# Optimization experiments

Measured on AMD Instinct MI355X. Metric: run time of the kernel, lower is better.

## Reference

```python
import jax, jax.numpy as jnp
import numpy as np

N = 100000
E = 1600000
F_IN = 512
HID = 64
N_CLASSES = 16


def setup_inputs() -> dict:
    key = jax.random.key(0)
    k0, k1, k2, k3 = jax.random.split(key, 4)
    features = jax.random.normal(k0, (N, F_IN), dtype=jnp.float32)
    edge_idx = jax.random.randint(k1, (2, E), 0, N, dtype=jnp.int64)
    # Glorot-style init matching torch_geometric GCNConv defaults
    W1 = jax.random.normal(k2, (F_IN, HID), dtype=jnp.float32) * (1.0 / np.sqrt(F_IN))
    b1 = jnp.zeros((HID,), dtype=jnp.float32)
    W2 = jax.random.normal(k3, (HID, N_CLASSES), dtype=jnp.float32) * (1.0 / np.sqrt(HID))
    b2 = jnp.zeros((N_CLASSES,), dtype=jnp.float32)
    return {"features": features, "edge_idx": edge_idx, "W1": W1, "b1": b1, "W2": W2, "b2": b2}


def _gcn_layer(x, row, col, norm, W, b):
    # Linear transform first (out_channels < in_channels -> cheaper messages)
    h = x @ W                                   # [N, out]
    msg = h[row] * norm[:, None]                # gather + scale, [E+N, out]
    out = jax.ops.segment_sum(msg, col, num_segments=x.shape[0])  # scatter-add
    return out + b


def reference(features, edge_idx, W1, b1, W2, b2):
    n = features.shape[0]
    loop = jnp.arange(n, dtype=edge_idx.dtype)
    row = jnp.concatenate([edge_idx[0], loop])  # sources (+ self-loops)
    col = jnp.concatenate([edge_idx[1], loop])  # targets (+ self-loops)
    w = jnp.ones(row.shape[0], dtype=features.dtype)  # edge_weight=None -> ones
    # Symmetric normalization D^{-1/2} A D^{-1/2} (degree over targets)
    deg = jax.ops.segment_sum(w, col, num_segments=n)
    dinv = jnp.where(deg > 0, deg ** -0.5, 0.0)
    norm = dinv[row] * w * dinv[col]            # [E+N]

    x = jax.nn.relu(_gcn_layer(features, row, col, norm, W1, b1))
    # Dropout: eval mode (identity)
    logits = _gcn_layer(x, row, col, norm, W2, b2)
    return logits
```

## Files before the change

kernel.cpp:

```cpp
#include <hip/hip_runtime.h>

#define NN 100000
#define EE 1600000
#define FIN 512
#define HID 64
#define NC 16
#define ELLW 64
#define CPAD 16

#define KB_ 196
#define BCAP 10240
#define S1E 2048

typedef __attribute__((ext_vector_type(8))) short bf16x8;
typedef __attribute__((ext_vector_type(4))) float f32x4;

__device__ __forceinline__ unsigned short f2bf(float f) {
    union { float f; unsigned u; } v; v.f = f;
    unsigned r = v.u + 0x7FFFu + ((v.u >> 16) & 1u);
    return (unsigned short)(r >> 16);
}
__device__ __forceinline__ float asf(unsigned u) {
    union { unsigned u; float f; } v; v.u = u; return v.f;
}

__global__ void k_zero(unsigned* __restrict__ p, int n) {
    int i = blockIdx.x * blockDim.x + threadIdx.x;
    if (i < n) p[i] = 0u;
}

__global__ __launch_bounds__(256) void k_bin(
    const int* __restrict__ erow, const int* __restrict__ ecol,
    unsigned* __restrict__ gcur, unsigned* __restrict__ staged) {
    __shared__ unsigned hist[256];
    __shared__ unsigned scanb[256];
    __shared__ unsigned cur[256];
    __shared__ unsigned sbase[256];
    __shared__ unsigned pk[S1E];
    __shared__ unsigned ga[S1E];
    const int t = threadIdx.x;
    const int e0 = blockIdx.x * S1E;

    hist[t] = 0;
    cur[t] = 0;
    __syncthreads();

    unsigned pkd[8];
    int bs[8];
#pragma unroll
    for (int i = 0; i < 8; ++i) {
        int e = e0 + i * 256 + t;
        if (e < EE) {
            int c = ecol[e];
            int src = erow[e];
            int b = c >> 9;
            bs[i] = b;
            pkd[i] = (unsigned)src | ((unsigned)(c & 511) << 17);
            atomicAdd(&hist[b], 1u);
        } else {
            bs[i] = -1;
        }
    }
    __syncthreads();
    scanb[t] = hist[t];
    __syncthreads();
    for (int d = 1; d < 256; d <<= 1) {
        unsigned add = (t >= d) ? scanb[t - d] : 0u;
        __syncthreads();
        scanb[t] += add;
        __syncthreads();
    }
    if (t < KB_ && hist[t] > 0) sbase[t] = atomicAdd(&gcur[(size_t)t * CPAD], hist[t]);
    __syncthreads();
#pragma unroll
    for (int i = 0; i < 8; ++i) {
        int b = bs[i];
        if (b >= 0) {
            unsigned ls = atomicAdd(&cur[b], 1u);
            unsigned pos = scanb[b] - hist[b] + ls;
            unsigned gp = sbase[b] + ls;
            pk[pos] = pkd[i];
            ga[pos] = (gp < BCAP) ? ((unsigned)b * BCAP + gp) : 0xFFFFFFFFu;
        }
    }
    __syncthreads();
    unsigned tot = scanb[255];
#pragma unroll
    for (int i = 0; i < 8; ++i) {
        unsigned idx = i * 256 + t;
        if (idx < tot && ga[idx] != 0xFFFFFFFFu) staged[ga[idx]] = pk[idx];
    }
}

__global__ __launch_bounds__(256) void k_scat2(
    const unsigned* __restrict__ gcur, const unsigned* __restrict__ staged,
    int* __restrict__ ell, unsigned* __restrict__ cnt, float* __restrict__ dinv) {
    __shared__ unsigned lcnt[512];
    const int t = threadIdx.x;
    const int b = blockIdx.x;
    lcnt[t] = 0; lcnt[t + 256] = 0;
    __syncthreads();
    unsigned n = gcur[(size_t)b * CPAD];
    if (n > BCAP) n = BCAP;
    const unsigned base = (unsigned)b * BCAP;
    const int node0 = b << 9;
    for (unsigned idx = t; idx < n; idx += 256) {
        unsigned p = staged[base + idx];
        int src = (int)(p & 0x1FFFFu);
        int dl = (int)(p >> 17);
        unsigned slot = atomicAdd(&lcnt[dl], 1u);
        if (slot < ELLW) ell[(size_t)(node0 + dl) * ELLW + slot] = src;
    }
    __syncthreads();
#pragma unroll
    for (int i = 0; i < 2; ++i) {
        int dl = i * 256 + t;
        int node = node0 + dl;
        if (node < NN) {
            unsigned c = lcnt[dl];
            cnt[node] = c;
            dinv[node] = 1.0f / sqrtf((float)(c + 1u));
        }
    }
}

__global__ void k_prepw(const float* __restrict__ W1, unsigned short* __restrict__ W1t) {
    int id = blockIdx.x * blockDim.x + threadIdx.x;
    if (id >= HID * FIN) return;
    int c = id >> 9;
    int k = id & 511;
    W1t[id] = f2bf(W1[(size_t)k * HID + c]);
}

#define BM 128
#define BK 64

__global__ __launch_bounds__(256) void k_gemm1(
    const float* __restrict__ A, const unsigned short* __restrict__ W1t,
    const float* __restrict__ dinv, unsigned short* __restrict__ h1s) {
    __shared__ unsigned short sA[BM * BK];
    __shared__ unsigned short sB[HID * BK];
    const int t = threadIdx.x;
    const int w = t >> 6;
    const int l = t & 63;
    const int row0 = blockIdx.x * BM;

    f32x4 acc[2][4];
#pragma unroll
    for (int fr = 0; fr < 2; ++fr)
#pragma unroll
        for (int fc = 0; fc < 4; ++fc)
            acc[fr][fc] = (f32x4){0.f, 0.f, 0.f, 0.f};

    for (int kb = 0; kb < FIN; kb += BK) {
        __syncthreads();
#pragma unroll
        for (int i = 0; i < 4; ++i) {
            int idx = i * 256 + t;
            int r = idx >> 3, g = idx & 7;
            float4 v0 = {0.f, 0.f, 0.f, 0.f}, v1 = {0.f, 0.f, 0.f, 0.f};
            if (row0 + r < NN) {
                const float* p = &A[(size_t)(row0 + r) * FIN + kb + g * 8];
                v0 = *reinterpret_cast<const float4*>(p);
                v1 = *reinterpret_cast<const float4*>(p + 4);
            }
            unsigned short tmp[8] = {f2bf(v0.x), f2bf(v0.y), f2bf(v0.z), f2bf(v0.w),
                                     f2bf(v1.x), f2bf(v1.y), f2bf(v1.z), f2bf(v1.w)};
            *reinterpret_cast<uint4*>((char*)sA + r * 128 + ((g ^ (r & 7)) << 4)) =
                *reinterpret_cast<uint4*>(tmp);
        }
#pragma unroll
        for (int i = 0; i < 2; ++i) {
            int idx = i * 256 + t;
            int c = idx >> 3, g = idx & 7;
            uint4 v = *reinterpret_cast<const uint4*>(&W1t[(size_t)c * FIN + kb + g * 8]);
            *reinterpret_cast<uint4*>((char*)sB + c * 128 + ((g ^ (c & 7)) << 4)) = v;
        }
        __syncthreads();
#pragma unroll
        for (int ks = 0; ks < 2; ++ks) {
            const int gk = ks * 4 + (l >> 4);
            bf16x8 a[2], b[4];
#pragma unroll
            for (int fr = 0; fr < 2; ++fr) {
                int r = w * 32 + fr * 16 + (l & 15);
                a[fr] = *reinterpret_cast<const bf16x8*>((char*)sA + r * 128 + ((gk ^ (r & 7)) << 4));
            }
#pragma unroll
            for (int fc = 0; fc < 4; ++fc) {
                int c = fc * 16 + (l & 15);
                b[fc] = *reinterpret_cast<const bf16x8*>((char*)sB + c * 128 + ((gk ^ (c & 7)) << 4));
            }
#pragma unroll
            for (int fr = 0; fr < 2; ++fr)
#pragma unroll
                for (int fc = 0; fc < 4; ++fc)
                    acc[fr][fc] = __builtin_amdgcn_mfma_f32_16x16x32_bf16(
                        a[fr], b[fc], acc[fr][fc], 0, 0, 0);
        }
    }
#pragma unroll
    for (int fr = 0; fr < 2; ++fr) {
#pragma unroll
        for (int r = 0; r < 4; ++r) {
            int grow = row0 + w * 32 + fr * 16 + (l >> 4) * 4 + r;
            if (grow >= NN) continue;
            float di = dinv[grow];
#pragma unroll
            for (int fc = 0; fc < 4; ++fc) {
                int col = fc * 16 + (l & 15);
                h1s[(size_t)grow * HID + col] = f2bf(acc[fr][fc][r] * di);
            }
        }
    }
}

__global__ __launch_bounds__(256) void k_agg1(
    const unsigned* __restrict__ cnt, const int* __restrict__ ell,
    const unsigned short* __restrict__ h1s, const float* __restrict__ dinv,
    const float* __restrict__ b1, unsigned short* __restrict__ x) {
    int wid = (blockIdx.x * blockDim.x + threadIdx.x) >> 6;
    if (wid >= NN) return;
    const int l = threadIdx.x & 63;
    const int g = l >> 3;
    const int q = l & 7;
    const int total = (int)cnt[wid] + 1;
    const int base = wid * ELLW;

    float a0 = 0.f, a1 = 0.f, a2 = 0.f, a3 = 0.f;
    float a4 = 0.f, a5 = 0.f, a6 = 0.f, a7 = 0.f;
    for (int s = 0; s < total; s += 8) {
        int e = s + g;
        int ee = min(e, total - 1);
        int src = (ee == 0) ? wid : ell[base + ee - 1];
        uint4 u = *reinterpret_cast<const uint4*>(&h1s[(size_t)src * HID + q * 8]);
        float m = (e < total) ? 1.f : 0.f;
        a0 = fmaf(m, asf(u.x << 16), a0);
        a1 = fmaf(m, asf(u.x & 0xFFFF0000u), a1);
        a2 = fmaf(m, asf(u.y << 16), a2);
        a3 = fmaf(m, asf(u.y & 0xFFFF0000u), a3);
        a4 = fmaf(m, asf(u.z << 16), a4);
        a5 = fmaf(m, asf(u.z & 0xFFFF0000u), a5);
        a6 = fmaf(m, asf(u.w << 16), a6);
        a7 = fmaf(m, asf(u.w & 0xFFFF0000u), a7);
    }
#pragma unroll
    for (int d = 8; d <= 32; d <<= 1) {
        a0 += __shfl_xor(a0, d); a1 += __shfl_xor(a1, d);
        a2 += __shfl_xor(a2, d); a3 += __shfl_xor(a3, d);
        a4 += __shfl_xor(a4, d); a5 += __shfl_xor(a5, d);
        a6 += __shfl_xor(a6, d); a7 += __shfl_xor(a7, d);
    }
    if (g == 0) {
        float di = dinv[wid];
        float4 bA = *reinterpret_cast<const float4*>(&b1[q * 8]);
        float4 bB = *reinterpret_cast<const float4*>(&b1[q * 8 + 4]);
        float r0 = fmaxf(fmaf(a0, di, bA.x), 0.f);
        float r1 = fmaxf(fmaf(a1, di, bA.y), 0.f);
        float r2 = fmaxf(fmaf(a2, di, bA.z), 0.f);
        float r3 = fmaxf(fmaf(a3, di, bA.w), 0.f);
        float r4 = fmaxf(fmaf(a4, di, bB.x), 0.f);
        float r5 = fmaxf(fmaf(a5, di, bB.y), 0.f);
        float r6 = fmaxf(fmaf(a6, di, bB.z), 0.f);
        float r7 = fmaxf(fmaf(a7, di, bB.w), 0.f);
        uint4 pv;
        pv.x = (unsigned)f2bf(r0) | ((unsigned)f2bf(r1) << 16);
        pv.y = (unsigned)f2bf(r2) | ((unsigned)f2bf(r3) << 16);
        pv.z = (unsigned)f2bf(r4) | ((unsigned)f2bf(r5) << 16);
        pv.w = (unsigned)f2bf(r6) | ((unsigned)f2bf(r7) << 16);
        *reinterpret_cast<uint4*>(&x[(size_t)wid * HID + q * 8]) = pv;
    }
}

__global__ __launch_bounds__(256) void k_gemm2(
    const unsigned short* __restrict__ x, const float* __restrict__ W2,
    const float* __restrict__ dinv, unsigned short* __restrict__ h2s) {
    __shared__ float sW[HID][NC];
    const int t = threadIdx.x;
#pragma unroll
    for (int i = 0; i < 4; ++i) {
        int q = t + i * 256;
        sW[q >> 4][q & 15] = W2[q];
    }
    __syncthreads();
    int i = blockIdx.x * blockDim.x + t;
    if (i >= NN) return;

    float acc[NC];
#pragma unroll
    for (int j = 0; j < NC; ++j) acc[j] = 0.f;
    const unsigned short* xr = &x[(size_t)i * HID];
#pragma unroll
    for (int k8 = 0; k8 < 8; ++k8) {
        uint4 u = *reinterpret_cast<const uint4*>(&xr[k8 * 8]);
        float f[8] = {asf(u.x << 16), asf(u.x & 0xFFFF0000u),
                      asf(u.y << 16), asf(u.y & 0xFFFF0000u),
                      asf(u.z << 16), asf(u.z & 0xFFFF0000u),
                      asf(u.w << 16), asf(u.w & 0xFFFF0000u)};
#pragma unroll
        for (int m = 0; m < 8; ++m)
#pragma unroll
            for (int j = 0; j < NC; ++j)
                acc[j] = fmaf(f[m], sW[k8 * 8 + m][j], acc[j]);
    }
    float di = dinv[i];
    unsigned short hv[NC];
#pragma unroll
    for (int j = 0; j < NC; ++j) hv[j] = f2bf(acc[j] * di);
    *reinterpret_cast<uint4*>(&h2s[(size_t)i * NC])     = *reinterpret_cast<uint4*>(hv);
    *reinterpret_cast<uint4*>(&h2s[(size_t)i * NC + 8]) = *reinterpret_cast<uint4*>(hv + 8);
}

__global__ __launch_bounds__(256) void k_agg2(
    const unsigned* __restrict__ cnt, const int* __restrict__ ell,
    const unsigned short* __restrict__ h2s, const float* __restrict__ dinv,
    const float* __restrict__ b2, float* __restrict__ out) {
    int wid = (blockIdx.x * blockDim.x + threadIdx.x) >> 6;
    if (wid >= NN) return;
    const int l = threadIdx.x & 63;
    const int g = l >> 1;
    const int q = l & 1;
    const int total = (int)cnt[wid] + 1;
    const int base = wid * ELLW;

    float a0 = 0.f, a1 = 0.f, a2 = 0.f, a3 = 0.f;
    float a4 = 0.f, a5 = 0.f, a6 = 0.f, a7 = 0.f;
    for (int s = 0; s < total; s += 32) {
        int e = s + g;
        int ee = min(e, total - 1);
        int src = (ee == 0) ? wid : ell[base + ee - 1];
        uint4 u = *reinterpret_cast<const uint4*>(&h2s[(size_t)src * NC + q * 8]);
        float m = (e < total) ? 1.f : 0.f;
        a0 = fmaf(m, asf(u.x << 16), a0);
        a1 = fmaf(m, asf(u.x & 0xFFFF0000u), a1);
        a2 = fmaf(m, asf(u.y << 16), a2);
        a3 = fmaf(m, asf(u.y & 0xFFFF0000u), a3);
        a4 = fmaf(m, asf(u.z << 16), a4);
        a5 = fmaf(m, asf(u.z & 0xFFFF0000u), a5);
        a6 = fmaf(m, asf(u.w << 16), a6);
        a7 = fmaf(m, asf(u.w & 0xFFFF0000u), a7);
    }
#pragma unroll
    for (int d = 2; d <= 32; d <<= 1) {
        a0 += __shfl_xor(a0, d); a1 += __shfl_xor(a1, d);
        a2 += __shfl_xor(a2, d); a3 += __shfl_xor(a3, d);
        a4 += __shfl_xor(a4, d); a5 += __shfl_xor(a5, d);
        a6 += __shfl_xor(a6, d); a7 += __shfl_xor(a7, d);
    }
    if (g == 0) {
        float di = dinv[wid];
        float4 bA = *reinterpret_cast<const float4*>(&b2[q * 8]);
        float4 bB = *reinterpret_cast<const float4*>(&b2[q * 8 + 4]);
        float4 w0, w1;
        w0.x = fmaf(a0, di, bA.x); w0.y = fmaf(a1, di, bA.y);
        w0.z = fmaf(a2, di, bA.z); w0.w = fmaf(a3, di, bA.w);
        w1.x = fmaf(a4, di, bB.x); w1.y = fmaf(a5, di, bB.y);
        w1.z = fmaf(a6, di, bB.z); w1.w = fmaf(a7, di, bB.w);
        *reinterpret_cast<float4*>(&out[(size_t)wid * NC + q * 8])     = w0;
        *reinterpret_cast<float4*>(&out[(size_t)wid * NC + q * 8 + 4]) = w1;
    }
}

extern "C" void kernel_launch(void* const* d_in, const int* in_sizes, int n_in,
                              void* d_out, int out_size, void* d_ws, size_t ws_size,
                              hipStream_t stream) {
    const float* features = (const float*)d_in[0];
    const int*   edges    = (const int*)d_in[1];
    const float* W1       = (const float*)d_in[2];
    const float* b1       = (const float*)d_in[3];
    const float* W2       = (const float*)d_in[4];
    const float* b2       = (const float*)d_in[5];
    float* out = (float*)d_out;

    const int* erow = edges;
    const int* ecol = edges + EE;

    char* ws = (char*)d_ws;
    size_t o = 0;
    auto alloc = [&](size_t bytes) { size_t p = o; o = (o + bytes + 255) & ~255ULL; return p; };
    unsigned*       gcur  = (unsigned*)      (ws + alloc((size_t)KB_ * CPAD * 4));
    unsigned*       cnt   = (unsigned*)      (ws + alloc((size_t)NN * 4));
    float*          dinv  = (float*)         (ws + alloc((size_t)NN * 4));
    unsigned*       staged= (unsigned*)      (ws + alloc((size_t)KB_ * BCAP * 4));
    unsigned short* W1t   = (unsigned short*)(ws + alloc((size_t)HID * FIN * 2));
    int*            ell   = (int*)           (ws + alloc((size_t)(KB_ << 9) * ELLW * 4));
    unsigned short* h1s   = (unsigned short*)(ws + alloc((size_t)NN * HID * 2));
    unsigned short* x     = (unsigned short*)(ws + alloc((size_t)NN * HID * 2));
    unsigned short* h2s   = (unsigned short*)(ws + alloc((size_t)NN * NC * 2));

    k_zero<<<(KB_ * CPAD + 255) / 256, 256, 0, stream>>>(gcur, KB_ * CPAD);
    k_prepw<<<(HID * FIN + 255) / 256, 256, 0, stream>>>(W1, W1t);
    k_bin<<<(EE + S1E - 1) / S1E, 256, 0, stream>>>(erow, ecol, gcur, staged);
    k_scat2<<<KB_, 256, 0, stream>>>(gcur, staged, ell, cnt, dinv);

    k_gemm1<<<(NN + BM - 1) / BM, 256, 0, stream>>>(features, W1t, dinv, h1s);
    k_agg1 <<<NN / 4, 256, 0, stream>>>(cnt, ell, h1s, dinv, b1, x);

    k_gemm2<<<(NN + 255) / 256, 256, 0, stream>>>(x, W2, dinv, h2s);
    k_agg2 <<<NN / 4, 256, 0, stream>>>(cnt, ell, h2s, dinv, b2, out);
}
```

Measured before the change: 188.2 us.

## Overlap GEMM1 with edge binning via heterogeneous fused launches

The source-side dinv scaling moves out of GEMM1 and into the aggregation gather, so GEMM1 no longer depends on the graph degree computation. GEMM1 blocks are then split across two launches that also run the binning and scatter stages, letting the feature GEMM overlap the graph-structure preprocessing. The zero and weight-prep kernels are merged into one init kernel. In exchange, agg1 does an extra dinv[src] load per edge, shared memory is sized for the larger of the two block bodies, and bf16 rounding of h1 now happens before the dinv scaling rather than after.

After: 198.6 us. +5.5%, slower.

```diff
diff --git a/kernel.cpp b/kernel.cpp
--- a/kernel.cpp
+++ b/kernel.cpp
@@ -11,6 +11,10 @@
 #define KB_ 196
 #define BCAP 10240
 #define S1E 2048
+#define NBIN 782
+#define GA 391
+#define GB 391
+#define SMEM_BYTES 24576
 
 typedef __attribute__((ext_vector_type(8))) short bf16x8;
 typedef __attribute__((ext_vector_type(4))) float f32x4;
@@ -24,126 +28,29 @@
     union { unsigned u; float f; } v; v.u = u; return v.f;
 }
 
-__global__ void k_zero(unsigned* __restrict__ p, int n) {
-    int i = blockIdx.x * blockDim.x + threadIdx.x;
-    if (i < n) p[i] = 0u;
-}
-
-__global__ __launch_bounds__(256) void k_bin(
-    const int* __restrict__ erow, const int* __restrict__ ecol,
-    unsigned* __restrict__ gcur, unsigned* __restrict__ staged) {
-    __shared__ unsigned hist[256];
-    __shared__ unsigned scanb[256];
-    __shared__ unsigned cur[256];
-    __shared__ unsigned sbase[256];
-    __shared__ unsigned pk[S1E];
-    __shared__ unsigned ga[S1E];
-    const int t = threadIdx.x;
-    const int e0 = blockIdx.x * S1E;
-
-    hist[t] = 0;
-    cur[t] = 0;
-    __syncthreads();
-
-    unsigned pkd[8];
-    int bs[8];
-#pragma unroll
-    for (int i = 0; i < 8; ++i) {
-        int e = e0 + i * 256 + t;
-        if (e < EE) {
-            int c = ecol[e];
-            int src = erow[e];
-            int b = c >> 9;
-            bs[i] = b;
-            pkd[i] = (unsigned)src | ((unsigned)(c & 511) << 17);
-            atomicAdd(&hist[b], 1u);
-        } else {
-            bs[i] = -1;
-        }
-    }
-    __syncthreads();
-    scanb[t] = hist[t];
-    __syncthreads();
-    for (int d = 1; d < 256; d <<= 1) {
-        unsigned add = (t >= d) ? scanb[t - d] : 0u;
-        __syncthreads();
-        scanb[t] += add;
-        __syncthreads();
-    }
-    if (t < KB_ && hist[t] > 0) sbase[t] = atomicAdd(&gcur[(size_t)t * CPAD], hist[t]);
-    __syncthreads();
-#pragma unroll
-    for (int i = 0; i < 8; ++i) {
-        int b = bs[i];
-        if (b >= 0) {
-            unsigned ls = atomicAdd(&cur[b], 1u);
-            unsigned pos = scanb[b] - hist[b] + ls;
-            unsigned gp = sbase[b] + ls;
-            pk[pos] = pkd[i];
-            ga[pos] = (gp < BCAP) ? ((unsigned)b * BCAP + gp) : 0xFFFFFFFFu;
-        }
-    }
-    __syncthreads();
-    unsigned tot = scanb[255];
-#pragma unroll
-    for (int i = 0; i < 8; ++i) {
-        unsigned idx = i * 256 + t;
-        if (idx < tot && ga[idx] != 0xFFFFFFFFu) staged[ga[idx]] = pk[idx];
-    }
-}
-
-__global__ __launch_bounds__(256) void k_scat2(
-    const unsigned* __restrict__ gcur, const unsigned* __restrict__ staged,
-    int* __restrict__ ell, unsigned* __restrict__ cnt, float* __restrict__ dinv) {
-    __shared__ unsigned lcnt[512];
-    const int t = threadIdx.x;
-    const int b = blockIdx.x;
-    lcnt[t] = 0; lcnt[t + 256] = 0;
-    __syncthreads();
-    unsigned n = gcur[(size_t)b * CPAD];
-    if (n > BCAP) n = BCAP;
-    const unsigned base = (unsigned)b * BCAP;
-    const int node0 = b << 9;
-    for (unsigned idx = t; idx < n; idx += 256) {
-        unsigned p = staged[base + idx];
-        int src = (int)(p & 0x1FFFFu);
-        int dl = (int)(p >> 17);
-        unsigned slot = atomicAdd(&lcnt[dl], 1u);
-        if (slot < ELLW) ell[(size_t)(node0 + dl) * ELLW + slot] = src;
-    }
-    __syncthreads();
-#pragma unroll
-    for (int i = 0; i < 2; ++i) {
-        int dl = i * 256 + t;
-        int node = node0 + dl;
-        if (node < NN) {
-            unsigned c = lcnt[dl];
-            cnt[node] = c;
-            dinv[node] = 1.0f / sqrtf((float)(c + 1u));
-        }
-    }
-}
-
-__global__ void k_prepw(const float* __restrict__ W1, unsigned short* __restrict__ W1t) {
+__global__ void k_init(const float* __restrict__ W1, unsigned short* __restrict__ W1t,
+                       unsigned* __restrict__ gcur) {
     int id = blockIdx.x * blockDim.x + threadIdx.x;
-    if (id >= HID * FIN) return;
-    int c = id >> 9;
-    int k = id & 511;
-    W1t[id] = f2bf(W1[(size_t)k * HID + c]);
+    if (id < KB_ * CPAD) gcur[id] = 0u;
+    if (id < HID * FIN) {
+        int c = id >> 9;
+        int k = id & 511;
+        W1t[id] = f2bf(W1[(size_t)k * HID + c]);
+    }
 }
 
 #define BM 128
 #define BK 64
 
-__global__ __launch_bounds__(256) void k_gemm1(
-    const float* __restrict__ A, const unsigned short* __restrict__ W1t,
-    const float* __restrict__ dinv, unsigned short* __restrict__ h1s) {
-    __shared__ unsigned short sA[BM * BK];
-    __shared__ unsigned short sB[HID * BK];
+__device__ __forceinline__ void gemm1_body(
+    char* smem, int blk, const float* __restrict__ A,
+    const unsigned short* __restrict__ W1t, unsigned short* __restrict__ h1s) {
+    unsigned short* sA = (unsigned short*)smem;
+    unsigned short* sB = (unsigned short*)(smem + BM * BK * 2);
     const int t = threadIdx.x;
     const int w = t >> 6;
     const int l = t & 63;
-    const int row0 = blockIdx.x * BM;
+    const int row0 = blk * BM;
 
     f32x4 acc[2][4];
 #pragma unroll
@@ -205,14 +112,127 @@
         for (int r = 0; r < 4; ++r) {
             int grow = row0 + w * 32 + fr * 16 + (l >> 4) * 4 + r;
             if (grow >= NN) continue;
-            float di = dinv[grow];
 #pragma unroll
             for (int fc = 0; fc < 4; ++fc) {
                 int col = fc * 16 + (l & 15);
-                h1s[(size_t)grow * HID + col] = f2bf(acc[fr][fc][r] * di);
+                h1s[(size_t)grow * HID + col] = f2bf(acc[fr][fc][r]);
             }
         }
     }
+}
+
+__device__ __forceinline__ void bin_body(
+    char* smem, int bb, const int* __restrict__ erow, const int* __restrict__ ecol,
+    unsigned* __restrict__ gcur, unsigned* __restrict__ staged) {
+    unsigned* hist  = (unsigned*)smem;
+    unsigned* scanb = hist + 256;
+    unsigned* cur   = scanb + 256;
+    unsigned* sbase = cur + 256;
+    unsigned* pk    = sbase + 256;
+    unsigned* ga    = pk + S1E;
+    const int t = threadIdx.x;
+    const int e0 = bb * S1E;
+
+    hist[t] = 0;
+    cur[t] = 0;
+    __syncthreads();
+
+    unsigned pkd[8];
+    int bs[8];
+#pragma unroll
+    for (int i = 0; i < 8; ++i) {
+        int e = e0 + i * 256 + t;
+        if (e < EE) {
+            int c = ecol[e];
+            int src = erow[e];
+            int b = c >> 9;
+            bs[i] = b;
+            pkd[i] = (unsigned)src | ((unsigned)(c & 511) << 17);
+            atomicAdd(&hist[b], 1u);
+        } else {
+            bs[i] = -1;
+        }
+    }
+    __syncthreads();
+    scanb[t] = hist[t];
+    __syncthreads();
+    for (int d = 1; d < 256; d <<= 1) {
+        unsigned add = (t >= d) ? scanb[t - d] : 0u;
+        __syncthreads();
+        scanb[t] += add;
+        __syncthreads();
+    }
+    if (t < KB_ && hist[t] > 0) sbase[t] = atomicAdd(&gcur[(size_t)t * CPAD], hist[t]);
+    __syncthreads();
+#pragma unroll
+    for (int i = 0; i < 8; ++i) {
+        int b = bs[i];
+        if (b >= 0) {
+            unsigned ls = atomicAdd(&cur[b], 1u);
+            unsigned pos = scanb[b] - hist[b] + ls;
+            unsigned gp = sbase[b] + ls;
+            pk[pos] = pkd[i];
+            ga[pos] = (gp < BCAP) ? ((unsigned)b * BCAP + gp) : 0xFFFFFFFFu;
+        }
+    }
+    __syncthreads();
+    unsigned tot = scanb[255];
+#pragma unroll
+    for (int i = 0; i < 8; ++i) {
+        unsigned idx = i * 256 + t;
+        if (idx < tot && ga[idx] != 0xFFFFFFFFu) staged[ga[idx]] = pk[idx];
+    }
+}
+
+__device__ __forceinline__ void scat2_body(
+    char* smem, int b, const unsigned* __restrict__ gcur, const unsigned* __restrict__ staged,
+    int* __restrict__ ell, unsigned* __restrict__ cnt, float* __restrict__ dinv) {
+    unsigned* lcnt = (unsigned*)smem;
+    const int t = threadIdx.x;
+    lcnt[t] = 0; lcnt[t + 256] = 0;
+    __syncthreads();
+    unsigned n = gcur[(size_t)b * CPAD];
+    if (n > BCAP) n = BCAP;
+    const unsigned base = (unsigned)b * BCAP;
+    const int node0 = b << 9;
+    for (unsigned idx = t; idx < n; idx += 256) {
+        unsigned p = staged[base + idx];
+        int src = (int)(p & 0x1FFFFu);
+        int dl = (int)(p >> 17);
+        unsigned slot = atomicAdd(&lcnt[dl], 1u);
+        if (slot < ELLW) ell[(size_t)(node0 + dl) * ELLW + slot] = src;
+    }
+    __syncthreads();
+#pragma unroll
+    for (int i = 0; i < 2; ++i) {
+        int dl = i * 256 + t;
+        int node = node0 + dl;
+        if (node < NN) {
+            unsigned c = lcnt[dl];
+            cnt[node] = c;
+            dinv[node] = 1.0f / sqrtf((float)(c + 1u));
+        }
+    }
+}
+
+__global__ __launch_bounds__(256) void k_phase1(
+    const float* __restrict__ A, const unsigned short* __restrict__ W1t,
+    unsigned short* __restrict__ h1s,
+    const int* __restrict__ erow, const int* __restrict__ ecol,
+    unsigned* __restrict__ gcur, unsigned* __restrict__ staged) {
+    extern __shared__ char smem[];
+    if (blockIdx.x < GA) gemm1_body(smem, blockIdx.x, A, W1t, h1s);
+    else                 bin_body(smem, blockIdx.x - GA, erow, ecol, gcur, staged);
+}
+
+__global__ __launch_bounds__(256) void k_phase2(
+    const float* __restrict__ A, const unsigned short* __restrict__ W1t,
+    unsigned short* __restrict__ h1s,
+    const unsigned* __restrict__ gcur, const unsigned* __restrict__ staged,
+    int* __restrict__ ell, unsigned* __restrict__ cnt, float* __restrict__ dinv) {
+    extern __shared__ char smem[];
+    if (blockIdx.x < GB) gemm1_body(smem, blockIdx.x + GA, A, W1t, h1s);
+    else                 scat2_body(smem, blockIdx.x - GB, gcur, staged, ell, cnt, dinv);
 }
 
 __global__ __launch_bounds__(256) void k_agg1(
@@ -234,7 +254,7 @@
         int ee = min(e, total - 1);
         int src = (ee == 0) ? wid : ell[base + ee - 1];
         uint4 u = *reinterpret_cast<const uint4*>(&h1s[(size_t)src * HID + q * 8]);
-        float m = (e < total) ? 1.f : 0.f;
+        float m = (e < total) ? dinv[src] : 0.f;
         a0 = fmaf(m, asf(u.x << 16), a0);
         a1 = fmaf(m, asf(u.x & 0xFFFF0000u), a1);
         a2 = fmaf(m, asf(u.y << 16), a2);
@@ -388,14 +408,10 @@
     unsigned short* x     = (unsigned short*)(ws + alloc((size_t)NN * HID * 2));
     unsigned short* h2s   = (unsigned short*)(ws + alloc((size_t)NN * NC * 2));
 
-    k_zero<<<(KB_ * CPAD + 255) / 256, 256, 0, stream>>>(gcur, KB_ * CPAD);
-    k_prepw<<<(HID * FIN + 255) / 256, 256, 0, stream>>>(W1, W1t);
-    k_bin<<<(EE + S1E - 1) / S1E, 256, 0, stream>>>(erow, ecol, gcur, staged);
-    k_scat2<<<KB_, 256, 0, stream>>>(gcur, staged, ell, cnt, dinv);
-
-    k_gemm1<<<(NN + BM - 1) / BM, 256, 0, stream>>>(features, W1t, dinv, h1s);
+    k_init<<<(HID * FIN + 255) / 256, 256, 0, stream>>>(W1, W1t, gcur);
+    k_phase1<<<GA + NBIN, 256, SMEM_BYTES, stream>>>(features, W1t, h1s, erow, ecol, gcur, staged);
+    k_phase2<<<GB + KB_, 256, SMEM_BYTES, stream>>>(features, W1t, h1s, gcur, staged, ell, cnt, dinv);
     k_agg1 <<<NN / 4, 256, 0, stream>>>(cnt, ell, h1s, dinv, b1, x);
-
     k_gemm2<<<(NN + 255) / 256, 256, 0, stream>>>(x, W2, dinv, h2s);
     k_agg2 <<<NN / 4, 256, 0, stream>>>(cnt, ell, h2s, dinv, b2, out);
 }
```

## Fuse layer-2 GEMM into layer-1 aggregation and shrink CSR bucket size

Applied to the files above, without the earlier changes.

Folds the small x@W2 projection into the layer-1 aggregation kernel. After the shuffle reduction each wave applies bias, ReLU and the 64x16 W2 product from shared memory and writes h2s directly, so the intermediate x buffer and one launch go away. It also merges the zero-init and W1 transpose kernels into one. The bucketing is halved to 256 nodes per bucket (391 buckets), so k_scat2 runs more blocks with one node per thread. The cost is extra shared-memory scan work in k_bin and tighter per-bucket staging capacity.

Result: slower. 203.6 us (+8.2%).

```diff
diff --git a/kernel.cpp b/kernel.cpp
--- a/kernel.cpp
+++ b/kernel.cpp
@@ -8,8 +8,8 @@
 #define ELLW 64
 #define CPAD 16
 
-#define KB_ 196
-#define BCAP 10240
+#define KB2 391
+#define BCAP2 4608
 #define S1E 2048
 
 typedef __attribute__((ext_vector_type(8))) short bf16x8;
@@ -24,25 +24,31 @@
     union { unsigned u; float f; } v; v.u = u; return v.f;
 }
 
-__global__ void k_zero(unsigned* __restrict__ p, int n) {
-    int i = blockIdx.x * blockDim.x + threadIdx.x;
-    if (i < n) p[i] = 0u;
+__global__ void k_init(const float* __restrict__ W1, unsigned short* __restrict__ W1t,
+                       unsigned* __restrict__ gcur) {
+    int id = blockIdx.x * blockDim.x + threadIdx.x;
+    if (id < KB2 * CPAD) gcur[id] = 0u;
+    if (id < HID * FIN) {
+        int c = id >> 9;
+        int k = id & 511;
+        W1t[id] = f2bf(W1[(size_t)k * HID + c]);
+    }
 }
 
 __global__ __launch_bounds__(256) void k_bin(
     const int* __restrict__ erow, const int* __restrict__ ecol,
     unsigned* __restrict__ gcur, unsigned* __restrict__ staged) {
-    __shared__ unsigned hist[256];
-    __shared__ unsigned scanb[256];
-    __shared__ unsigned cur[256];
-    __shared__ unsigned sbase[256];
+    __shared__ unsigned hist[512];
+    __shared__ unsigned scanb[512];
+    __shared__ unsigned cur[512];
+    __shared__ unsigned sbase[512];
     __shared__ unsigned pk[S1E];
     __shared__ unsigned ga[S1E];
     const int t = threadIdx.x;
     const int e0 = blockIdx.x * S1E;
 
-    hist[t] = 0;
-    cur[t] = 0;
+    hist[t] = 0; hist[t + 256] = 0;
+    cur[t] = 0;  cur[t + 256] = 0;
     __syncthreads();
 
     unsigned pkd[8];
@@ -53,9 +59,9 @@
         if (e < EE) {
             int c = ecol[e];
             int src = erow[e];
-            int b = c >> 9;
+            int b = c >> 8;
             bs[i] = b;
-            pkd[i] = (unsigned)src | ((unsigned)(c & 511) << 17);
+            pkd[i] = (unsigned)src | ((unsigned)(c & 255) << 17);
             atomicAdd(&hist[b], 1u);
         } else {
             bs[i] = -1;
@@ -63,14 +69,24 @@
     }
     __syncthreads();
     scanb[t] = hist[t];
+    scanb[t + 256] = hist[t + 256];
     __syncthreads();
     for (int d = 1; d < 256; d <<= 1) {
-        unsigned add = (t >= d) ? scanb[t - d] : 0u;
+        unsigned aA = (t >= d) ? scanb[t - d] : 0u;
+        unsigned aB = (t >= d) ? scanb[256 + t - d] : 0u;
         __syncthreads();
-        scanb[t] += add;
+        scanb[t] += aA;
+        scanb[256 + t] += aB;
         __syncthreads();
     }
-    if (t < KB_ && hist[t] > 0) sbase[t] = atomicAdd(&gcur[(size_t)t * CPAD], hist[t]);
+    unsigned totA = scanb[255];
+    scanb[256 + t] += totA;
+    __syncthreads();
+    if (hist[t] > 0) sbase[t] = atomicAdd(&gcur[(size_t)t * CPAD], hist[t]);
+    {
+        int t2 = t + 256;
+        if (t2 < KB2 && hist[t2] > 0) sbase[t2] = atomicAdd(&gcur[(size_t)t2 * CPAD], hist[t2]);
+    }
     __syncthreads();
 #pragma unroll
     for (int i = 0; i < 8; ++i) {
@@ -80,11 +96,11 @@
             unsigned pos = scanb[b] - hist[b] + ls;
             unsigned gp = sbase[b] + ls;
             pk[pos] = pkd[i];
-            ga[pos] = (gp < BCAP) ? ((unsigned)b * BCAP + gp) : 0xFFFFFFFFu;
-        }
-    }
-    __syncthreads();
-    unsigned tot = scanb[255];
+            ga[pos] = (gp < BCAP2) ? ((unsigned)b * BCAP2 + gp) : 0xFFFFFFFFu;
+        }
+    }
+    __syncthreads();
+    unsigned tot = scanb[511];
 #pragma unroll
     for (int i = 0; i < 8; ++i) {
         unsigned idx = i * 256 + t;
@@ -95,15 +111,15 @@
 __global__ __launch_bounds__(256) void k_scat2(
     const unsigned* __restrict__ gcur, const unsigned* __restrict__ staged,
     int* __restrict__ ell, unsigned* __restrict__ cnt, float* __restrict__ dinv) {
-    __shared__ unsigned lcnt[512];
+    __shared__ unsigned lcnt[256];
     const int t = threadIdx.x;
     const int b = blockIdx.x;
-    lcnt[t] = 0; lcnt[t + 256] = 0;
+    lcnt[t] = 0;
     __syncthreads();
     unsigned n = gcur[(size_t)b * CPAD];
-    if (n > BCAP) n = BCAP;
-    const unsigned base = (unsigned)b * BCAP;
-    const int node0 = b << 9;
+    if (n > BCAP2) n = BCAP2;
+    const unsigned base = (unsigned)b * BCAP2;
+    const int node0 = b << 8;
     for (unsigned idx = t; idx < n; idx += 256) {
         unsigned p = staged[base + idx];
         int src = (int)(p & 0x1FFFFu);
@@ -112,24 +128,12 @@
         if (slot < ELLW) ell[(size_t)(node0 + dl) * ELLW + slot] = src;
     }
     __syncthreads();
-#pragma unroll
-    for (int i = 0; i < 2; ++i) {
-        int dl = i * 256 + t;
-        int node = node0 + dl;
-        if (node < NN) {
-            unsigned c = lcnt[dl];
-            cnt[node] = c;
-            dinv[node] = 1.0f / sqrtf((float)(c + 1u));
-        }
-    }
-}
-
-__global__ void k_prepw(const float* __restrict__ W1, unsigned short* __restrict__ W1t) {
-    int id = blockIdx.x * blockDim.x + threadIdx.x;
-    if (id >= HID * FIN) return;
-    int c = id >> 9;
-    int k = id & 511;
-    W1t[id] = f2bf(W1[(size_t)k * HID + c]);
+    int node = node0 + t;
+    if (node < NN) {
+        unsigned c = lcnt[t];
+        cnt[node] = c;
+        dinv[node] = 1.0f / sqrtf((float)(c + 1u));
+    }
 }
 
 #define BM 128
@@ -215,13 +219,25 @@
     }
 }
 
-__global__ __launch_bounds__(256) void k_agg1(
+__global__ __launch_bounds__(256) void k_agg1f(
     const unsigned* __restrict__ cnt, const int* __restrict__ ell,
     const unsigned short* __restrict__ h1s, const float* __restrict__ dinv,
-    const float* __restrict__ b1, unsigned short* __restrict__ x) {
-    int wid = (blockIdx.x * blockDim.x + threadIdx.x) >> 6;
+    const float* __restrict__ b1, const float* __restrict__ W2,
+    unsigned short* __restrict__ h2s) {
+    __shared__ float sW2[HID][NC + 1];
+    __shared__ float sb1[HID];
+    const int t = threadIdx.x;
+#pragma unroll
+    for (int i = 0; i < 4; ++i) {
+        int idx = i * 256 + t;
+        sW2[idx >> 4][idx & 15] = W2[idx];
+    }
+    if (t < HID) sb1[t] = b1[t];
+    __syncthreads();
+
+    int wid = (blockIdx.x * blockDim.x + t) >> 6;
     if (wid >= NN) return;
-    const int l = threadIdx.x & 63;
+    const int l = t & 63;
     const int g = l >> 3;
     const int q = l & 7;
     const int total = (int)cnt[wid] + 1;
@@ -251,64 +267,30 @@
         a4 += __shfl_xor(a4, d); a5 += __shfl_xor(a5, d);
         a6 += __shfl_xor(a6, d); a7 += __shfl_xor(a7, d);
     }
-    if (g == 0) {
-        float di = dinv[wid];
-        float4 bA = *reinterpret_cast<const float4*>(&b1[q * 8]);
-        float4 bB = *reinterpret_cast<const float4*>(&b1[q * 8 + 4]);
-        float r0 = fmaxf(fmaf(a0, di, bA.x), 0.f);
-        float r1 = fmaxf(fmaf(a1, di, bA.y), 0.f);
-        float r2 = fmaxf(fmaf(a2, di, bA.z), 0.f);
-        float r3 = fmaxf(fmaf(a3, di, bA.w), 0.f);
-        float r4 = fmaxf(fmaf(a4, di, bB.x), 0.f);
-        float r5 = fmaxf(fmaf(a5, di, bB.y), 0.f);
-        float r6 = fmaxf(fmaf(a6, di, bB.z), 0.f);
-        float r7 = fmaxf(fmaf(a7, di, bB.w), 0.f);
-        uint4 pv;
-        pv.x = (unsigned)f2bf(r0) | ((unsigned)f2bf(r1) << 16);
-        pv.y = (unsigned)f2bf(r2) | ((unsigned)f2bf(r3) << 16);
-        pv.z = (unsigned)f2bf(r4) | ((unsigned)f2bf(r5) << 16);
-        pv.w = (unsigned)f2bf(r6) | ((unsigned)f2bf(r7) << 16);
-        *reinterpret_cast<uint4*>(&x[(size_t)wid * HID + q * 8]) = pv;
-    }
-}
-
-__global__ __launch_bounds__(256) void k_gemm2(
-    const unsigned short* __restrict__ x, const float* __restrict__ W2,
-    const float* __restrict__ dinv, unsigned short* __restrict__ h2s) {
-    __shared__ float sW[HID][NC];
-    const int t = threadIdx.x;
-#pragma unroll
-    for (int i = 0; i < 4; ++i) {
-        int q = t + i * 256;
-        sW[q >> 4][q & 15] = W2[q];
-    }
-    __syncthreads();
-    int i = blockIdx.x * blockDim.x + t;
-    if (i >= NN) return;
-
-    float acc[NC];
-#pragma unroll
-    for (int j = 0; j < NC; ++j) acc[j] = 0.f;
-    const unsigned short* xr = &x[(size_t)i * HID];
-#pragma unroll
-    for (int k8 = 0; k8 < 8; ++k8) {
-        uint4 u = *reinterpret_cast<const uint4*>(&xr[k8 * 8]);
-        float f[8] = {asf(u.x << 16), asf(u.x & 0xFFFF0000u),
-                      asf(u.y << 16), asf(u.y & 0xFFFF0000u),
-                      asf(u.z << 16), asf(u.z & 0xFFFF0000u),
-                      asf(u.w << 16), asf(u.w & 0xFFFF0000u)};
-#pragma unroll
-        for (int m = 0; m < 8; ++m)
-#pragma unroll
-            for (int j = 0; j < NC; ++j)
-                acc[j] = fmaf(f[m], sW[k8 * 8 + m][j], acc[j]);
-    }
-    float di = dinv[i];
-    unsigned short hv[NC];
-#pragma unroll
-    for (int j = 0; j < NC; ++j) hv[j] = f2bf(acc[j] * di);
-    *reinterpret_cast<uint4*>(&h2s[(size_t)i * NC])     = *reinterpret_cast<uint4*>(hv);
-    *reinterpret_cast<uint4*>(&h2s[(size_t)i * NC + 8]) = *reinterpret_cast<uint4*>(hv + 8);
+    const float di = dinv[wid];
+    const int ch0 = q * 8;
+    float x0 = fmaxf(fmaf(a0, di, sb1[ch0 + 0]), 0.f);
+    float x1 = fmaxf(fmaf(a1, di, sb1[ch0 + 1]), 0.f);
+    float x2 = fmaxf(fmaf(a2, di, sb1[ch0 + 2]), 0.f);
+    float x3 = fmaxf(fmaf(a3, di, sb1[ch0 + 3]), 0.f);
+    float x4 = fmaxf(fmaf(a4, di, sb1[ch0 + 4]), 0.f);
+    float x5 = fmaxf(fmaf(a5, di, sb1[ch0 + 5]), 0.f);
+    float x6 = fmaxf(fmaf(a6, di, sb1[ch0 + 6]), 0.f);
+    float x7 = fmaxf(fmaf(a7, di, sb1[ch0 + 7]), 0.f);
+    const int c0 = 2 * g, c1 = 2 * g + 1;
+    float p0 = x0 * sW2[ch0 + 0][c0] + x1 * sW2[ch0 + 1][c0] + x2 * sW2[ch0 + 2][c0] +
+               x3 * sW2[ch0 + 3][c0] + x4 * sW2[ch0 + 4][c0] + x5 * sW2[ch0 + 5][c0] +
+               x6 * sW2[ch0 + 6][c0] + x7 * sW2[ch0 + 7][c0];
+    float p1 = x0 * sW2[ch0 + 0][c1] + x1 * sW2[ch0 + 1][c1] + x2 * sW2[ch0 + 2][c1] +
+               x3 * sW2[ch0 + 3][c1] + x4 * sW2[ch0 + 4][c1] + x5 * sW2[ch0 + 5][c1] +
+               x6 * sW2[ch0 + 6][c1] + x7 * sW2[ch0 + 7][c1];
+    p0 += __shfl_xor(p0, 1); p1 += __shfl_xor(p1, 1);
+    p0 += __shfl_xor(p0, 2); p1 += __shfl_xor(p1, 2);
+    p0 += __shfl_xor(p0, 4); p1 += __shfl_xor(p1, 4);
+    if (q == 0) {
+        unsigned u = (unsigned)f2bf(p0 * di) | ((unsigned)f2bf(p1 * di) << 16);
+        *reinterpret_cast<unsigned*>(&h2s[(size_t)wid * NC + c0]) = u;
+    }
 }
 
 __global__ __launch_bounds__(256) void k_agg2(
@@ -378,24 +360,19 @@
     char* ws = (char*)d_ws;
     size_t o = 0;
     auto alloc = [&](size_t bytes) { size_t p = o; o = (o + bytes + 255) & ~255ULL; return p; };
-    unsigned*       gcur  = (unsigned*)      (ws + alloc((size_t)KB_ * CPAD * 4));
+    unsigned*       gcur  = (unsigned*)      (ws + alloc((size_t)KB2 * CPAD * 4));
     unsigned*       cnt   = (unsigned*)      (ws + alloc((size_t)NN * 4));
     float*          dinv  = (float*)         (ws + alloc((size_t)NN * 4));
-    unsigned*       staged= (unsigned*)      (ws + alloc((size_t)KB_ * BCAP * 4));
+    unsigned*       staged= (unsigned*)      (ws + alloc((size_t)KB2 * BCAP2 * 4));
     unsigned short* W1t   = (unsigned short*)(ws + alloc((size_t)HID * FIN * 2));
-    int*            ell   = (int*)           (ws + alloc((size_t)(KB_ << 9) * ELLW * 4));
+    int*            ell   = (int*)           (ws + alloc((size_t)(KB2 << 8) * ELLW * 4));
     unsigned short* h1s   = (unsigned short*)(ws + alloc((size_t)NN * HID * 2));
-    unsigned short* x     = (unsigned short*)(ws + alloc((size_t)NN * HID * 2));
     unsigned short* h2s   = (unsigned short*)(ws + alloc((size_t)NN * NC * 2));
 
-    k_zero<<<(KB_ * CPAD + 255) / 256, 256, 0, stream>>>(gcur, KB_ * CPAD);
-    k_prepw<<<(HID * FIN + 255) / 256, 256, 0, stream>>>(W1, W1t);
-    k_bin<<<(EE + S1E - 1) / S1E, 256, 0, stream>>>(erow, ecol, gcur, staged);
-    k_scat2<<<KB_, 256, 0, stream>>>(gcur, staged, ell, cnt, dinv);
-
+    k_init <<<128, 256, 0, stream>>>(W1, W1t, gcur);
+    k_bin  <<<(EE + S1E - 1) / S1E, 256, 0, stream>>>(erow, ecol, gcur, staged);
+    k_scat2<<<KB2, 256, 0, stream>>>(gcur, staged, ell, cnt, dinv);
     k_gemm1<<<(NN + BM - 1) / BM, 256, 0, stream>>>(features, W1t, dinv, h1s);
-    k_agg1 <<<NN / 4, 256, 0, stream>>>(cnt, ell, h1s, dinv, b1, x);
-
-    k_gemm2<<<(NN + 255) / 256, 256, 0, stream>>>(x, W2, dinv, h2s);
+    k_agg1f<<<NN / 4, 256, 0, stream>>>(cnt, ell, h1s, dinv, b1, W2, h2s);
     k_agg2 <<<NN / 4, 256, 0, stream>>>(cnt, ell, h2s, dinv, b2, out);
 }
```

## Halve bucket width, stage ELL rows in LDS, and merge init kernels

Applied to the files above, without the earlier changes.

Bins edges into 391 destination buckets of 256 nodes instead of 196 of 512, extending the block-local scan to 512 entries. The ELL build now runs two blocks per bucket, each handling 128 nodes. Each block assembles its rows in a padded LDS tile and writes them out coalesced, replacing scattered global stores. The zeroing and weight-conversion kernels are merged into one launch. This raises parallelism in the graph build and removes a launch, at the cost of each bucket's staged edges being read twice and a smaller per-bucket overflow capacity.

Measured after the change: 193.8 us. 1.03x slower.

```diff
diff --git a/kernel.cpp b/kernel.cpp
--- a/kernel.cpp
+++ b/kernel.cpp
@@ -8,8 +8,8 @@
 #define ELLW 64
 #define CPAD 16
 
-#define KB_ 196
-#define BCAP 10240
+#define KB2 391
+#define BCAP2 4608
 #define S1E 2048
 
 typedef __attribute__((ext_vector_type(8))) short bf16x8;
@@ -24,25 +24,31 @@
     union { unsigned u; float f; } v; v.u = u; return v.f;
 }
 
-__global__ void k_zero(unsigned* __restrict__ p, int n) {
-    int i = blockIdx.x * blockDim.x + threadIdx.x;
-    if (i < n) p[i] = 0u;
+__global__ void k_init(const float* __restrict__ W1, unsigned short* __restrict__ W1t,
+                       unsigned* __restrict__ gcur) {
+    int id = blockIdx.x * blockDim.x + threadIdx.x;
+    if (id < KB2 * CPAD) gcur[id] = 0u;
+    if (id < HID * FIN) {
+        int c = id >> 9;
+        int k = id & 511;
+        W1t[id] = f2bf(W1[(size_t)k * HID + c]);
+    }
 }
 
 __global__ __launch_bounds__(256) void k_bin(
     const int* __restrict__ erow, const int* __restrict__ ecol,
     unsigned* __restrict__ gcur, unsigned* __restrict__ staged) {
-    __shared__ unsigned hist[256];
-    __shared__ unsigned scanb[256];
-    __shared__ unsigned cur[256];
-    __shared__ unsigned sbase[256];
+    __shared__ unsigned hist[512];
+    __shared__ unsigned scanb[512];
+    __shared__ unsigned cur[512];
+    __shared__ unsigned sbase[512];
     __shared__ unsigned pk[S1E];
     __shared__ unsigned ga[S1E];
     const int t = threadIdx.x;
     const int e0 = blockIdx.x * S1E;
 
-    hist[t] = 0;
-    cur[t] = 0;
+    hist[t] = 0; hist[t + 256] = 0;
+    cur[t] = 0;  cur[t + 256] = 0;
     __syncthreads();
 
     unsigned pkd[8];
@@ -53,9 +59,9 @@
         if (e < EE) {
             int c = ecol[e];
             int src = erow[e];
-            int b = c >> 9;
+            int b = c >> 8;
             bs[i] = b;
-            pkd[i] = (unsigned)src | ((unsigned)(c & 511) << 17);
+            pkd[i] = (unsigned)src | ((unsigned)(c & 255) << 17);
             atomicAdd(&hist[b], 1u);
         } else {
             bs[i] = -1;
@@ -63,14 +69,24 @@
     }
     __syncthreads();
     scanb[t] = hist[t];
+    scanb[t + 256] = hist[t + 256];
     __syncthreads();
     for (int d = 1; d < 256; d <<= 1) {
-        unsigned add = (t >= d) ? scanb[t - d] : 0u;
+        unsigned aA = (t >= d) ? scanb[t - d] : 0u;
+        unsigned aB = (t >= d) ? scanb[256 + t - d] : 0u;
         __syncthreads();
-        scanb[t] += add;
+        scanb[t] += aA;
+        scanb[256 + t] += aB;
         __syncthreads();
     }
-    if (t < KB_ && hist[t] > 0) sbase[t] = atomicAdd(&gcur[(size_t)t * CPAD], hist[t]);
+    unsigned totA = scanb[255];
+    scanb[256 + t] += totA;
+    __syncthreads();
+    if (hist[t] > 0) sbase[t] = atomicAdd(&gcur[(size_t)t * CPAD], hist[t]);
+    {
+        int t2 = t + 256;
+        if (t2 < KB2 && hist[t2] > 0) sbase[t2] = atomicAdd(&gcur[(size_t)t2 * CPAD], hist[t2]);
+    }
     __syncthreads();
 #pragma unroll
     for (int i = 0; i < 8; ++i) {
@@ -80,11 +96,11 @@
             unsigned pos = scanb[b] - hist[b] + ls;
             unsigned gp = sbase[b] + ls;
             pk[pos] = pkd[i];
-            ga[pos] = (gp < BCAP) ? ((unsigned)b * BCAP + gp) : 0xFFFFFFFFu;
-        }
-    }
-    __syncthreads();
-    unsigned tot = scanb[255];
+            ga[pos] = (gp < BCAP2) ? ((unsigned)b * BCAP2 + gp) : 0xFFFFFFFFu;
+        }
+    }
+    __syncthreads();
+    unsigned tot = scanb[511];
 #pragma unroll
     for (int i = 0; i < 8; ++i) {
         unsigned idx = i * 256 + t;
@@ -95,41 +111,42 @@
 __global__ __launch_bounds__(256) void k_scat2(
     const unsigned* __restrict__ gcur, const unsigned* __restrict__ staged,
     int* __restrict__ ell, unsigned* __restrict__ cnt, float* __restrict__ dinv) {
-    __shared__ unsigned lcnt[512];
+    __shared__ int tile[128 * 65];
+    __shared__ unsigned lcnt[128];
     const int t = threadIdx.x;
-    const int b = blockIdx.x;
-    lcnt[t] = 0; lcnt[t + 256] = 0;
+    const int b = blockIdx.x >> 1;
+    const int dl0 = (blockIdx.x & 1) << 7;
+    if (t < 128) lcnt[t] = 0;
     __syncthreads();
     unsigned n = gcur[(size_t)b * CPAD];
-    if (n > BCAP) n = BCAP;
-    const unsigned base = (unsigned)b * BCAP;
-    const int node0 = b << 9;
+    if (n > BCAP2) n = BCAP2;
+    const unsigned base = (unsigned)b * BCAP2;
     for (unsigned idx = t; idx < n; idx += 256) {
         unsigned p = staged[base + idx];
-        int src = (int)(p & 0x1FFFFu);
-        int dl = (int)(p >> 17);
-        unsigned slot = atomicAdd(&lcnt[dl], 1u);
-        if (slot < ELLW) ell[(size_t)(node0 + dl) * ELLW + slot] = src;
-    }
-    __syncthreads();
-#pragma unroll
-    for (int i = 0; i < 2; ++i) {
-        int dl = i * 256 + t;
-        int node = node0 + dl;
-        if (node < NN) {
-            unsigned c = lcnt[dl];
+        int dl = (int)(p >> 17) - dl0;
+        if ((unsigned)dl < 128u) {
+            int src = (int)(p & 0x1FFFFu);
+            unsigned slot = atomicAdd(&lcnt[dl], 1u);
+            if (slot < ELLW) tile[dl * 65 + slot] = src;
+        }
+    }
+    __syncthreads();
+    const int node0 = (b << 8) + dl0;
+    int nrows = NN - node0;
+    if (nrows > 128) nrows = 128;
+    if (nrows > 0) {
+        int* eout = ell + (size_t)node0 * ELLW;
+        for (int i = t; i < nrows * ELLW; i += 256) {
+            int row = i >> 6, col = i & 63;
+            eout[i] = tile[row * 65 + col];
+        }
+        if (t < nrows) {
+            int node = node0 + t;
+            unsigned c = lcnt[t];
             cnt[node] = c;
             dinv[node] = 1.0f / sqrtf((float)(c + 1u));
         }
     }
-}
-
-__global__ void k_prepw(const float* __restrict__ W1, unsigned short* __restrict__ W1t) {
-    int id = blockIdx.x * blockDim.x + threadIdx.x;
-    if (id >= HID * FIN) return;
-    int c = id >> 9;
-    int k = id & 511;
-    W1t[id] = f2bf(W1[(size_t)k * HID + c]);
 }
 
 #define BM 128
@@ -378,24 +395,21 @@
     char* ws = (char*)d_ws;
     size_t o = 0;
     auto alloc = [&](size_t bytes) { size_t p = o; o = (o + bytes + 255) & ~255ULL; return p; };
-    unsigned*       gcur  = (unsigned*)      (ws + alloc((size_t)KB_ * CPAD * 4));
+    unsigned*       gcur  = (unsigned*)      (ws + alloc((size_t)KB2 * CPAD * 4));
     unsigned*       cnt   = (unsigned*)      (ws + alloc((size_t)NN * 4));
     float*          dinv  = (float*)         (ws + alloc((size_t)NN * 4));
-    unsigned*       staged= (unsigned*)      (ws + alloc((size_t)KB_ * BCAP * 4));
+    unsigned*       staged= (unsigned*)      (ws + alloc((size_t)KB2 * BCAP2 * 4));
     unsigned short* W1t   = (unsigned short*)(ws + alloc((size_t)HID * FIN * 2));
-    int*            ell   = (int*)           (ws + alloc((size_t)(KB_ << 9) * ELLW * 4));
+    int*            ell   = (int*)           (ws + alloc((size_t)(KB2 << 8) * ELLW * 4));
     unsigned short* h1s   = (unsigned short*)(ws + alloc((size_t)NN * HID * 2));
     unsigned short* x     = (unsigned short*)(ws + alloc((size_t)NN * HID * 2));
     unsigned short* h2s   = (unsigned short*)(ws + alloc((size_t)NN * NC * 2));
 
-    k_zero<<<(KB_ * CPAD + 255) / 256, 256, 0, stream>>>(gcur, KB_ * CPAD);
-    k_prepw<<<(HID * FIN + 255) / 256, 256, 0, stream>>>(W1, W1t);
-    k_bin<<<(EE + S1E - 1) / S1E, 256, 0, stream>>>(erow, ecol, gcur, staged);
-    k_scat2<<<KB_, 256, 0, stream>>>(gcur, staged, ell, cnt, dinv);
-
+    k_init <<<128, 256, 0, stream>>>(W1, W1t, gcur);
+    k_bin  <<<(EE + S1E - 1) / S1E, 256, 0, stream>>>(erow, ecol, gcur, staged);
+    k_scat2<<<KB2 * 2, 256, 0, stream>>>(gcur, staged, ell, cnt, dinv);
     k_gemm1<<<(NN + BM - 1) / BM, 256, 0, stream>>>(features, W1t, dinv, h1s);
     k_agg1 <<<NN / 4, 256, 0, stream>>>(cnt, ell, h1s, dinv, b1, x);
-
     k_gemm2<<<(NN + 255) / 256, 256, 0, stream>>>(x, W2, dinv, h2s);
     k_agg2 <<<NN / 4, 256, 0, stream>>>(cnt, ell, h2s, dinv, b2, out);
 }
```
